# Optimization experiments

Hardware: AMD Instinct MI355X
Metric: run time of the kernel (lower is better)

## Reference

```python
import jax, jax.numpy as jnp
import numpy as np

B, S, D, L, K, N = 2048, 50, 64, 500, 4, 100000
LN_EPS = 1e-12
TAU = 0.1


def _layernorm(x, w, b):
    m = x.mean(-1, keepdims=True)
    v = ((x - m) ** 2).mean(-1, keepdims=True)
    return (x - m) / jnp.sqrt(v + LN_EPS) * w + b


def _l2norm(x):
    n = jnp.linalg.norm(x, axis=-1, keepdims=True)
    return x / jnp.maximum(n, 1e-12)


def setup_inputs() -> dict:
    key = jax.random.key(0)
    ks = jax.random.split(key, 10)
    item_seq = jax.random.randint(ks[0], (B, S), 0, N, dtype=jnp.int64)
    item_seq_len = jax.random.randint(ks[1], (B,), 1, S + 1, dtype=jnp.int64)
    init = 0.01
    item_emb = jax.random.normal(ks[2], (N, D), jnp.float32) * 0.05
    item_emb = item_emb.at[0].set(0.0)  # padding_idx=0
    C = jax.random.normal(ks[3], (L, D), jnp.float32) * 0.05
    w1 = jax.random.normal(ks[4], (D, D), jnp.float32) * init
    w2 = jax.random.normal(ks[5], (D,), jnp.float32) * init
    w3 = jax.random.normal(ks[6], (D, D), jnp.float32) * init
    w4 = jax.random.normal(ks[7], (D,), jnp.float32) * init
    w_k_1 = jax.random.normal(ks[8], (K, D, D), jnp.float32) * init
    w_k_2 = jax.random.normal(ks[9], (K, D), jnp.float32) * init
    ln2_w = jnp.ones((D,), jnp.float32); ln2_b = jnp.zeros((D,), jnp.float32)
    ln4_w = jnp.ones((D,), jnp.float32); ln4_b = jnp.zeros((D,), jnp.float32)
    return {"item_seq": item_seq, "item_seq_len": item_seq_len,
            "item_emb": item_emb, "C": C, "w1": w1, "w2": w2, "w3": w3,
            "w4": w4, "w_k_1": w_k_1, "w_k_2": w_k_2,
            "ln2_w": ln2_w, "ln2_b": ln2_b, "ln4_w": ln4_w, "ln4_b": ln4_b}


def reference(item_seq, item_seq_len, item_emb, C, w1, w2, w3, w4,
              w_k_1, w_k_2, ln2_w, ln2_b, ln4_w, ln4_b):
    del item_seq_len  # unused by the original forward
    x_u = item_emb[item_seq]                                   # [B,S,D]
    x = jnp.tanh(x_u @ w1) @ w2                                # [B,S]
    a = jax.nn.softmax(x, axis=1)                              # attention over seq
    z_u = jnp.einsum('bs,bsd->bd', a, x_u)                     # [B,D]
    s_u = z_u @ C.T                                            # [B,L] prototype scores
    # top-k prototypes kept in ASCENDING order (argsort then last k), as in torch
    idx = jnp.argsort(s_u, axis=1)[:, -K:]                     # [B,K]
    s_top = jnp.sort(s_u, axis=1)[:, -K:]                      # [B,K]
    c_u = C[idx]                                               # [B,K,D] gather
    C_u = c_u * jax.nn.sigmoid(s_top)[..., None]               # [B,K,D]
    w3_x_u_norm = _l2norm(x_u @ w3)                            # [B,S,D]
    C_u_norm = _layernorm(C_u, ln2_w, ln2_b)                   # [B,K,D]
    P_k_t = jnp.einsum('bsd,bkd->bsk', w3_x_u_norm, C_u_norm)  # [B,S,K]
    P_k_t_b = jax.nn.softmax(P_k_t, axis=2)                    # over interests
    # per-interest position attention
    a_k = jnp.einsum('bsd,kde->bkse', x_u, w_k_1)              # [B,K,S,D]
    P_t_k = jax.nn.softmax(jnp.einsum('bkse,ke->bks', jnp.tanh(a_k), w_k_2), axis=2)
    mul_p = jnp.transpose(P_k_t_b, (0, 2, 1)) * P_t_k          # [B,K,S]
    delta_k = _l2norm(jnp.einsum('bks,bsd->bkd', mul_p, x_u))  # [B,K,D]
    x_u_bar = jnp.einsum('bsk,bkd->bsd', P_k_t_b, C_u)         # [B,S,D]
    C_apt = jax.nn.softmax(jnp.tanh(x_u_bar @ w3) @ w4, axis=1)  # [B,S]
    C_apt = jnp.einsum('bs,bsd->bd', C_apt, x_u_bar)           # [B,D]
    C_apt = _layernorm(C_apt, ln4_w, ln4_b)                    # [B,D]
    e_k = jnp.einsum('bkd,bd->bk', delta_k, C_apt) / TAU       # [B,K]
    e_k_u = jax.nn.softmax(e_k, axis=1)
    v_u = jnp.einsum('bk,bkd->bd', e_k_u, delta_k)             # [B,D]
    scores = v_u @ item_emb.T                                  # [B,N]
    return scores
```

## Files before the change

kernel.cpp:

```cpp
#include <hip/hip_runtime.h>
#include <cmath>

#define NB 2048
#define SS 50
#define DD 64
#define LL 500
#define KP 4
#define NI 100000

__device__ __forceinline__ float wsum(float v) {
#pragma unroll
    for (int m = 32; m >= 1; m >>= 1) v += __shfl_xor(v, m, 64);
    return v;
}
__device__ __forceinline__ float wmax(float v) {
#pragma unroll
    for (int m = 32; m >= 1; m >>= 1) v = fmaxf(v, __shfl_xor(v, m, 64));
    return v;
}

__device__ __forceinline__ void proj_logits(const float* xin,
                                            const float* __restrict__ W,
                                            const float* __restrict__ wv,
                                            float* lg, int wave, int lane) {
    float acc[13];
#pragma unroll
    for (int i = 0; i < 13; i++) acc[i] = 0.f;
#pragma unroll 1
    for (int dc = 0; dc < DD; dc += 8) {
        float wr[8];
#pragma unroll
        for (int t = 0; t < 8; t++) wr[t] = W[(dc + t) * DD + lane];
#pragma unroll
        for (int i = 0; i < 13; i++) {
            int s = wave + 4 * i;
            if (s < SS) {
                const float4* xr = reinterpret_cast<const float4*>(xin + s * DD + dc);
#pragma unroll
                for (int q = 0; q < 2; q++) {
                    float4 xv = xr[q];
                    acc[i] = fmaf(xv.x, wr[4 * q + 0], acc[i]);
                    acc[i] = fmaf(xv.y, wr[4 * q + 1], acc[i]);
                    acc[i] = fmaf(xv.z, wr[4 * q + 2], acc[i]);
                    acc[i] = fmaf(xv.w, wr[4 * q + 3], acc[i]);
                }
            }
        }
    }
    float wl = wv[lane];
#pragma unroll
    for (int i = 0; i < 13; i++) {
        int s = wave + 4 * i;
        if (s < SS) {
            float v = tanhf(acc[i]) * wl;
            v = wsum(v);
            if (lane == 0) lg[s] = v;
        }
    }
}

__global__ __launch_bounds__(256, 3) void sine_main(
    const int* __restrict__ item_seq,
    const float* __restrict__ emb,
    const float* __restrict__ Cm,
    const float* __restrict__ w1, const float* __restrict__ w2,
    const float* __restrict__ w3, const float* __restrict__ w4,
    const float* __restrict__ wk1, const float* __restrict__ wk2,
    const float* __restrict__ ln2w, const float* __restrict__ ln2b,
    const float* __restrict__ ln4w, const float* __restrict__ ln4b,
    float* __restrict__ vu_out) {
    __shared__ float xu[SS][DD];
    __shared__ float su[LL];
    __shared__ float lg[SS];
    __shared__ float aw[SS];
    __shared__ float zu[DD];
    __shared__ float cu[KP][DD];
    __shared__ float cun[KP][DD];
    __shared__ float pkt[SS][KP];
    __shared__ float ptk[KP][SS];
    __shared__ float dlt[KP][DD];
    __shared__ float capt[DD];
    __shared__ float eks[KP];
    __shared__ int sidx[SS];
    __shared__ int tidx[KP];
    __shared__ float tval[KP];

    const int tid = threadIdx.x, wave = tid >> 6, lane = tid & 63;
    const int b = blockIdx.x;

    if (tid < SS) sidx[tid] = item_seq[b * SS + tid];
    __syncthreads();

    for (int i = tid; i < SS * (DD / 4); i += 256) {
        int s = i >> 4, c = i & 15;
        float4 v = reinterpret_cast<const float4*>(emb + (size_t)sidx[s] * DD)[c];
        reinterpret_cast<float4*>(&xu[s][0])[c] = v;
    }
    __syncthreads();

    proj_logits(&xu[0][0], w1, w2, lg, wave, lane);
    __syncthreads();
    if (wave == 0) {
        float v = (lane < SS) ? lg[lane] : -INFINITY;
        float mx = wmax(v);
        float e = (lane < SS) ? expf(v - mx) : 0.f;
        float sm = wsum(e);
        if (lane < SS) aw[lane] = e / sm;
    }
    __syncthreads();

    if (tid < DD) {
        float z = 0.f;
        for (int s = 0; s < SS; s++) z = fmaf(aw[s], xu[s][tid], z);
        zu[tid] = z;
    }
    __syncthreads();

    for (int l = tid; l < LL; l += 256) {
        const float* cr = Cm + (size_t)l * DD;
        float a0 = 0.f;
        for (int d = 0; d < DD; d++) a0 = fmaf(zu[d], cr[d], a0);
        su[l] = a0;
    }
    __syncthreads();

    for (int p = 0; p < KP; p++) {
        float bv = -INFINITY;
        int bi = -1;
        for (int l = lane; l < LL; l += 64) {
            float v = su[l];
            if (v > bv || (v == bv && l > bi)) { bv = v; bi = l; }
        }
#pragma unroll
        for (int m = 32; m >= 1; m >>= 1) {
            float ov = __shfl_xor(bv, m, 64);
            int oi = __shfl_xor(bi, m, 64);
            if (ov > bv || (ov == bv && oi > bi)) { bv = ov; bi = oi; }
        }
        if (tid == 0) { tidx[KP - 1 - p] = bi; tval[KP - 1 - p] = bv; su[bi] = -INFINITY; }
        __syncthreads();
    }

    {
        int k = wave;
        float sv = tval[k];
        float sg = 1.f / (1.f + expf(-sv));
        float c = Cm[(size_t)tidx[k] * DD + lane] * sg;
        cu[k][lane] = c;
        float mean = wsum(c) * (1.f / DD);
        float dv = c - mean;
        float var = wsum(dv * dv) * (1.f / DD);
        float nv = dv / sqrtf(var + 1e-12f);
        cun[k][lane] = nv * ln2w[lane] + ln2b[lane];
    }
    __syncthreads();

    {
        float acc[13];
#pragma unroll
        for (int i = 0; i < 13; i++) acc[i] = 0.f;
#pragma unroll 1
        for (int dc = 0; dc < DD; dc += 8) {
            float wr[8];
#pragma unroll
            for (int t = 0; t < 8; t++) wr[t] = w3[(dc + t) * DD + lane];
#pragma unroll
            for (int i = 0; i < 13; i++) {
                int s = wave + 4 * i;
                if (s < SS) {
                    const float4* xr = reinterpret_cast<const float4*>(&xu[s][dc]);
#pragma unroll
                    for (int q = 0; q < 2; q++) {
                        float4 xv = xr[q];
                        acc[i] = fmaf(xv.x, wr[4 * q + 0], acc[i]);
                        acc[i] = fmaf(xv.y, wr[4 * q + 1], acc[i]);
                        acc[i] = fmaf(xv.z, wr[4 * q + 2], acc[i]);
                        acc[i] = fmaf(xv.w, wr[4 * q + 3], acc[i]);
                    }
                }
            }
        }
#pragma unroll
        for (int i = 0; i < 13; i++) {
            int s = wave + 4 * i;
            if (s < SS) {
                float y = acc[i];
                float n2 = wsum(y * y);
                float yn = y / fmaxf(sqrtf(n2), 1e-12f);
                float p0 = wsum(yn * cun[0][lane]);
                float p1 = wsum(yn * cun[1][lane]);
                float p2 = wsum(yn * cun[2][lane]);
                float p3 = wsum(yn * cun[3][lane]);
                if (lane == 0) {
                    float mx = fmaxf(fmaxf(p0, p1), fmaxf(p2, p3));
                    float e0 = expf(p0 - mx), e1 = expf(p1 - mx);
                    float e2 = expf(p2 - mx), e3 = expf(p3 - mx);
                    float sm = e0 + e1 + e2 + e3;
                    pkt[s][0] = e0 / sm; pkt[s][1] = e1 / sm;
                    pkt[s][2] = e2 / sm; pkt[s][3] = e3 / sm;
                }
            }
        }
    }
    __syncthreads();

    {
        int k = wave;
        const float* Wk = wk1 + (size_t)k * DD * DD;
        float wl = wk2[k * DD + lane];
#pragma unroll 1
        for (int sc = 0; sc < SS; sc += 10) {
            float acc[10];
#pragma unroll
            for (int i = 0; i < 10; i++) acc[i] = 0.f;
#pragma unroll 1
            for (int dc = 0; dc < DD; dc += 8) {
                float wr[8];
#pragma unroll
                for (int t = 0; t < 8; t++) wr[t] = Wk[(dc + t) * DD + lane];
#pragma unroll
                for (int i = 0; i < 10; i++) {
                    const float4* xr = reinterpret_cast<const float4*>(&xu[sc + i][dc]);
#pragma unroll
                    for (int q = 0; q < 2; q++) {
                        float4 xv = xr[q];
                        acc[i] = fmaf(xv.x, wr[4 * q + 0], acc[i]);
                        acc[i] = fmaf(xv.y, wr[4 * q + 1], acc[i]);
                        acc[i] = fmaf(xv.z, wr[4 * q + 2], acc[i]);
                        acc[i] = fmaf(xv.w, wr[4 * q + 3], acc[i]);
                    }
                }
            }
#pragma unroll
            for (int i = 0; i < 10; i++) {
                float v = tanhf(acc[i]) * wl;
                v = wsum(v);
                if (lane == 0) ptk[k][sc + i] = v;
            }
        }
    }
    __syncthreads();
    {
        int k = wave;
        float v = (lane < SS) ? ptk[k][lane] : -INFINITY;
        float mx = wmax(v);
        float e = (lane < SS) ? expf(v - mx) : 0.f;
        float sm = wsum(e);
        if (lane < SS) ptk[k][lane] = e / sm;
    }
    __syncthreads();

    {
        int k = wave;
        float a0 = 0.f;
        for (int s = 0; s < SS; s++) {
            float m = pkt[s][k] * ptk[k][s];
            a0 = fmaf(m, xu[s][lane], a0);
        }
        float n2 = wsum(a0 * a0);
        dlt[k][lane] = a0 / fmaxf(sqrtf(n2), 1e-12f);
    }
    __syncthreads();

    for (int i = tid; i < SS * DD; i += 256) {
        int s = i >> 6, d = i & 63;
        xu[s][d] = pkt[s][0] * cu[0][d] + pkt[s][1] * cu[1][d] +
                   pkt[s][2] * cu[2][d] + pkt[s][3] * cu[3][d];
    }
    __syncthreads();

    proj_logits(&xu[0][0], w3, w4, lg, wave, lane);
    __syncthreads();
    if (wave == 0) {
        float v = (lane < SS) ? lg[lane] : -INFINITY;
        float mx = wmax(v);
        float e = (lane < SS) ? expf(v - mx) : 0.f;
        float sm = wsum(e);
        if (lane < SS) aw[lane] = e / sm;
    }
    __syncthreads();
    if (tid < DD) {
        float z = 0.f;
        for (int s = 0; s < SS; s++) z = fmaf(aw[s], xu[s][tid], z);
        float mean = wsum(z) * (1.f / DD);
        float dv = z - mean;
        float var = wsum(dv * dv) * (1.f / DD);
        capt[tid] = dv / sqrtf(var + 1e-12f) * ln4w[tid] + ln4b[tid];
    }
    __syncthreads();

    {
        int k = wave;
        float v = dlt[k][lane] * capt[lane];
        v = wsum(v);
        if (lane == 0) eks[k] = v * 10.f;
    }
    __syncthreads();
    if (tid < DD) {
        float e0 = eks[0], e1 = eks[1], e2 = eks[2], e3 = eks[3];
        float mx = fmaxf(fmaxf(e0, e1), fmaxf(e2, e3));
        float x0 = expf(e0 - mx), x1 = expf(e1 - mx);
        float x2 = expf(e2 - mx), x3 = expf(e3 - mx);
        float sm = x0 + x1 + x2 + x3;
        float vu = (x0 * dlt[0][tid] + x1 * dlt[1][tid] +
                    x2 * dlt[2][tid] + x3 * dlt[3][tid]) / sm;
        vu_out[(size_t)b * DD + tid] = vu;
    }
}

__global__ __launch_bounds__(256) void sine_scores(const float* __restrict__ vu,
                                                   const float* __restrict__ emb,
                                                   float* __restrict__ out) {
    const int btile = blockIdx.x;
    const int n = blockIdx.y * 256 + threadIdx.x;
    if (n >= NI) return;
    float acc[32];
#pragma unroll
    for (int i = 0; i < 32; i++) acc[i] = 0.f;
    const float4* er = reinterpret_cast<const float4*>(emb + (size_t)n * DD);
    const float* vb = vu + (size_t)btile * 32 * DD;
#pragma unroll
    for (int dc = 0; dc < 16; dc++) {
        float4 e = er[dc];
#pragma unroll
        for (int i = 0; i < 32; i++) {
            const float* vr = vb + i * DD + dc * 4;
            acc[i] = fmaf(e.x, vr[0], acc[i]);
            acc[i] = fmaf(e.y, vr[1], acc[i]);
            acc[i] = fmaf(e.z, vr[2], acc[i]);
            acc[i] = fmaf(e.w, vr[3], acc[i]);
        }
    }
    size_t base = (size_t)btile * 32 * NI + n;
#pragma unroll
    for (int i = 0; i < 32; i++) out[base + (size_t)i * NI] = acc[i];
}

extern "C" void kernel_launch(void* const* d_in, const int* in_sizes, int n_in,
                              void* d_out, int out_size, void* d_ws, size_t ws_size,
                              hipStream_t stream) {
    const int* item_seq = (const int*)d_in[0];
    const float* emb = (const float*)d_in[2];
    const float* Cm = (const float*)d_in[3];
    const float* w1 = (const float*)d_in[4];
    const float* w2 = (const float*)d_in[5];
    const float* w3 = (const float*)d_in[6];
    const float* w4 = (const float*)d_in[7];
    const float* wk1 = (const float*)d_in[8];
    const float* wk2 = (const float*)d_in[9];
    const float* ln2w = (const float*)d_in[10];
    const float* ln2b = (const float*)d_in[11];
    const float* ln4w = (const float*)d_in[12];
    const float* ln4b = (const float*)d_in[13];
    float* out = (float*)d_out;
    float* vu = (float*)d_ws;

    sine_main<<<NB, 256, 0, stream>>>(item_seq, emb, Cm, w1, w2, w3, w4,
                                      wk1, wk2, ln2w, ln2b, ln4w, ln4b, vu);
    dim3 g2(NB / 32, (NI + 255) / 256);
    sine_scores<<<g2, 256, 0, stream>>>(vu, emb, out);
}
```

Measured before the change: 1.300 ms.

## Widen main kernel to 512 threads and double batch tile in scores GEMM

Launches the per-user main kernel with 8 waves instead of 4, redistributing sequence rows across waves, splitting the per-interest projection across two waves per interest, and computing prototype scores with a wave-parallel dot product over coalesced rows of C. The scores kernel now computes 64 users per thread instead of 32, halving the number of re-reads of the embedding table at the cost of 64 accumulators per thread and more register pressure. The aim is more latency hiding in the main kernel and less memory traffic in the large output GEMM.

```diff
diff --git a/kernel.cpp b/kernel.cpp
--- a/kernel.cpp
+++ b/kernel.cpp
@@ -19,21 +19,21 @@
     return v;
 }
 
-__device__ __forceinline__ void proj_logits(const float* xin,
-                                            const float* __restrict__ W,
-                                            const float* __restrict__ wv,
-                                            float* lg, int wave, int lane) {
-    float acc[13];
-#pragma unroll
-    for (int i = 0; i < 13; i++) acc[i] = 0.f;
+__device__ __forceinline__ void proj_logits8(const float* xin,
+                                             const float* __restrict__ W,
+                                             const float* __restrict__ wv,
+                                             float* lg, int wave, int lane) {
+    float acc[7];
+#pragma unroll
+    for (int i = 0; i < 7; i++) acc[i] = 0.f;
 #pragma unroll 1
     for (int dc = 0; dc < DD; dc += 8) {
         float wr[8];
 #pragma unroll
         for (int t = 0; t < 8; t++) wr[t] = W[(dc + t) * DD + lane];
 #pragma unroll
-        for (int i = 0; i < 13; i++) {
-            int s = wave + 4 * i;
+        for (int i = 0; i < 7; i++) {
+            int s = wave + 8 * i;
             if (s < SS) {
                 const float4* xr = reinterpret_cast<const float4*>(xin + s * DD + dc);
 #pragma unroll
@@ -49,8 +49,8 @@
     }
     float wl = wv[lane];
 #pragma unroll
-    for (int i = 0; i < 13; i++) {
-        int s = wave + 4 * i;
+    for (int i = 0; i < 7; i++) {
+        int s = wave + 8 * i;
         if (s < SS) {
             float v = tanhf(acc[i]) * wl;
             v = wsum(v);
@@ -59,7 +59,7 @@
     }
 }
 
-__global__ __launch_bounds__(256, 3) void sine_main(
+__global__ __launch_bounds__(512, 4) void sine_main(
     const int* __restrict__ item_seq,
     const float* __restrict__ emb,
     const float* __restrict__ Cm,
@@ -91,14 +91,14 @@
     if (tid < SS) sidx[tid] = item_seq[b * SS + tid];
     __syncthreads();
 
-    for (int i = tid; i < SS * (DD / 4); i += 256) {
+    for (int i = tid; i < SS * (DD / 4); i += 512) {
         int s = i >> 4, c = i & 15;
         float4 v = reinterpret_cast<const float4*>(emb + (size_t)sidx[s] * DD)[c];
         reinterpret_cast<float4*>(&xu[s][0])[c] = v;
     }
     __syncthreads();
 
-    proj_logits(&xu[0][0], w1, w2, lg, wave, lane);
+    proj_logits8(&xu[0][0], w1, w2, lg, wave, lane);
     __syncthreads();
     if (wave == 0) {
         float v = (lane < SS) ? lg[lane] : -INFINITY;
@@ -116,11 +116,13 @@
     }
     __syncthreads();
 
-    for (int l = tid; l < LL; l += 256) {
-        const float* cr = Cm + (size_t)l * DD;
-        float a0 = 0.f;
-        for (int d = 0; d < DD; d++) a0 = fmaf(zu[d], cr[d], a0);
-        su[l] = a0;
+    {
+        float zr = zu[lane];
+        for (int l = wave; l < LL; l += 8) {
+            float c = Cm[(size_t)l * DD + lane];
+            float v = wsum(zr * c);
+            if (lane == 0) su[l] = v;
+        }
     }
     __syncthreads();
 
@@ -141,7 +143,7 @@
         __syncthreads();
     }
 
-    {
+    if (wave < KP) {
         int k = wave;
         float sv = tval[k];
         float sg = 1.f / (1.f + expf(-sv));
@@ -156,17 +158,17 @@
     __syncthreads();
 
     {
-        float acc[13];
-#pragma unroll
-        for (int i = 0; i < 13; i++) acc[i] = 0.f;
+        float acc[7];
+#pragma unroll
+        for (int i = 0; i < 7; i++) acc[i] = 0.f;
 #pragma unroll 1
         for (int dc = 0; dc < DD; dc += 8) {
             float wr[8];
 #pragma unroll
             for (int t = 0; t < 8; t++) wr[t] = w3[(dc + t) * DD + lane];
 #pragma unroll
-            for (int i = 0; i < 13; i++) {
-                int s = wave + 4 * i;
+            for (int i = 0; i < 7; i++) {
+                int s = wave + 8 * i;
                 if (s < SS) {
                     const float4* xr = reinterpret_cast<const float4*>(&xu[s][dc]);
 #pragma unroll
@@ -181,8 +183,8 @@
             }
         }
 #pragma unroll
-        for (int i = 0; i < 13; i++) {
-            int s = wave + 4 * i;
+        for (int i = 0; i < 7; i++) {
+            int s = wave + 8 * i;
             if (s < SS) {
                 float y = acc[i];
                 float n2 = wsum(y * y);
@@ -205,42 +207,48 @@
     __syncthreads();
 
     {
-        int k = wave;
+        int k = wave >> 1, half = wave & 1;
         const float* Wk = wk1 + (size_t)k * DD * DD;
         float wl = wk2[k * DD + lane];
 #pragma unroll 1
-        for (int sc = 0; sc < SS; sc += 10) {
-            float acc[10];
-#pragma unroll
-            for (int i = 0; i < 10; i++) acc[i] = 0.f;
+        for (int c = 0; c < 2; c++) {
+            int sbase = half * 25 + c * 13;
+            int nr = c ? 12 : 13;
+            float acc[13];
+#pragma unroll
+            for (int i = 0; i < 13; i++) acc[i] = 0.f;
 #pragma unroll 1
             for (int dc = 0; dc < DD; dc += 8) {
                 float wr[8];
 #pragma unroll
                 for (int t = 0; t < 8; t++) wr[t] = Wk[(dc + t) * DD + lane];
 #pragma unroll
-                for (int i = 0; i < 10; i++) {
-                    const float4* xr = reinterpret_cast<const float4*>(&xu[sc + i][dc]);
-#pragma unroll
-                    for (int q = 0; q < 2; q++) {
-                        float4 xv = xr[q];
-                        acc[i] = fmaf(xv.x, wr[4 * q + 0], acc[i]);
-                        acc[i] = fmaf(xv.y, wr[4 * q + 1], acc[i]);
-                        acc[i] = fmaf(xv.z, wr[4 * q + 2], acc[i]);
-                        acc[i] = fmaf(xv.w, wr[4 * q + 3], acc[i]);
+                for (int i = 0; i < 13; i++) {
+                    if (i < nr) {
+                        const float4* xr = reinterpret_cast<const float4*>(&xu[sbase + i][dc]);
+#pragma unroll
+                        for (int q = 0; q < 2; q++) {
+                            float4 xv = xr[q];
+                            acc[i] = fmaf(xv.x, wr[4 * q + 0], acc[i]);
+                            acc[i] = fmaf(xv.y, wr[4 * q + 1], acc[i]);
+                            acc[i] = fmaf(xv.z, wr[4 * q + 2], acc[i]);
+                            acc[i] = fmaf(xv.w, wr[4 * q + 3], acc[i]);
+                        }
                     }
                 }
             }
 #pragma unroll
-            for (int i = 0; i < 10; i++) {
-                float v = tanhf(acc[i]) * wl;
-                v = wsum(v);
-                if (lane == 0) ptk[k][sc + i] = v;
-            }
-        }
-    }
-    __syncthreads();
-    {
+            for (int i = 0; i < 13; i++) {
+                if (i < nr) {
+                    float v = tanhf(acc[i]) * wl;
+                    v = wsum(v);
+                    if (lane == 0) ptk[k][sbase + i] = v;
+                }
+            }
+        }
+    }
+    __syncthreads();
+    if (wave < KP) {
         int k = wave;
         float v = (lane < SS) ? ptk[k][lane] : -INFINITY;
         float mx = wmax(v);
@@ -250,7 +258,7 @@
     }
     __syncthreads();
 
-    {
+    if (wave < KP) {
         int k = wave;
         float a0 = 0.f;
         for (int s = 0; s < SS; s++) {
@@ -262,14 +270,14 @@
     }
     __syncthreads();
 
-    for (int i = tid; i < SS * DD; i += 256) {
+    for (int i = tid; i < SS * DD; i += 512) {
         int s = i >> 6, d = i & 63;
         xu[s][d] = pkt[s][0] * cu[0][d] + pkt[s][1] * cu[1][d] +
                    pkt[s][2] * cu[2][d] + pkt[s][3] * cu[3][d];
     }
     __syncthreads();
 
-    proj_logits(&xu[0][0], w3, w4, lg, wave, lane);
+    proj_logits8(&xu[0][0], w3, w4, lg, wave, lane);
     __syncthreads();
     if (wave == 0) {
         float v = (lane < SS) ? lg[lane] : -INFINITY;
@@ -289,7 +297,7 @@
     }
     __syncthreads();
 
-    {
+    if (wave < KP) {
         int k = wave;
         float v = dlt[k][lane] * capt[lane];
         v = wsum(v);
@@ -308,22 +316,22 @@
     }
 }
 
-__global__ __launch_bounds__(256) void sine_scores(const float* __restrict__ vu,
-                                                   const float* __restrict__ emb,
-                                                   float* __restrict__ out) {
+__global__ __launch_bounds__(256, 4) void sine_scores(const float* __restrict__ vu,
+                                                      const float* __restrict__ emb,
+                                                      float* __restrict__ out) {
     const int btile = blockIdx.x;
     const int n = blockIdx.y * 256 + threadIdx.x;
     if (n >= NI) return;
-    float acc[32];
-#pragma unroll
-    for (int i = 0; i < 32; i++) acc[i] = 0.f;
+    float acc[64];
+#pragma unroll
+    for (int i = 0; i < 64; i++) acc[i] = 0.f;
     const float4* er = reinterpret_cast<const float4*>(emb + (size_t)n * DD);
-    const float* vb = vu + (size_t)btile * 32 * DD;
+    const float* vb = vu + (size_t)btile * 64 * DD;
 #pragma unroll
     for (int dc = 0; dc < 16; dc++) {
         float4 e = er[dc];
 #pragma unroll
-        for (int i = 0; i < 32; i++) {
+        for (int i = 0; i < 64; i++) {
             const float* vr = vb + i * DD + dc * 4;
             acc[i] = fmaf(e.x, vr[0], acc[i]);
             acc[i] = fmaf(e.y, vr[1], acc[i]);
@@ -331,9 +339,9 @@
             acc[i] = fmaf(e.w, vr[3], acc[i]);
         }
     }
-    size_t base = (size_t)btile * 32 * NI + n;
-#pragma unroll
-    for (int i = 0; i < 32; i++) out[base + (size_t)i * NI] = acc[i];
+    size_t base = (size_t)btile * 64 * NI + n;
+#pragma unroll
+    for (int i = 0; i < 64; i++) out[base + (size_t)i * NI] = acc[i];
 }
 
 extern "C" void kernel_launch(void* const* d_in, const int* in_sizes, int n_in,
@@ -355,8 +363,8 @@
     float* out = (float*)d_out;
     float* vu = (float*)d_ws;
 
-    sine_main<<<NB, 256, 0, stream>>>(item_seq, emb, Cm, w1, w2, w3, w4,
+    sine_main<<<NB, 512, 0, stream>>>(item_seq, emb, Cm, w1, w2, w3, w4,
                                       wk1, wk2, ln2w, ln2b, ln4w, ln4b, vu);
-    dim3 g2(NB / 32, (NI + 255) / 256);
+    dim3 g2(NB / 64, (NI + 255) / 256);
     sine_scores<<<g2, 256, 0, stream>>>(vu, emb, out);
 }
```

Measured after the change: 1.416 ms. 8.9% more time.
